# Optimization experiments

Hardware: AMD Instinct MI355X
Metric: run time of the kernel (lower is better)

Reference implementation:

```python
import jax, jax.numpy as jnp
import numpy as np

N_OUT, D_OUT, N_IN, D_IN, N_ROUTING = 32, 32, 2048, 16, 3
BATCH = 64


def squash(x, axis=-1):
    norm2 = jnp.sum(x * x, axis=axis, keepdims=True)
    scale = norm2 / (1.0 + norm2) / jnp.sqrt(norm2)
    return scale * x


def setup_inputs() -> dict:
    key = jax.random.key(0)
    k_u, k_w = jax.random.split(key)
    u = jax.random.normal(k_u, (BATCH, N_IN, D_IN), dtype=jnp.float32)
    stdv = 1.0 / np.sqrt(N_IN)
    W = jax.random.uniform(k_w, (N_IN, D_IN, N_OUT * D_OUT), dtype=jnp.float32,
                           minval=-stdv, maxval=stdv)
    return {"u": u, "W": W}


def reference(u, W):
    B = u.shape[0]
    # uhat[b,n,o,k] = sum_i u[b,n,i] * W[n,i,o*k]
    uhat = jnp.einsum('bni,nij->bnj', u, W).reshape(B, N_IN, N_OUT, D_OUT)
    b = jnp.zeros((B, N_IN, N_OUT), dtype=u.dtype)
    v = None
    for r in range(N_ROUTING):
        c = jax.nn.softmax(b, axis=-1)            # [B, nIn, nOut]
        s = jnp.einsum('bno,bnok->bok', c, uhat)  # [B, nOut, dOut]
        v = squash(s)
        if r != N_ROUTING - 1:
            a = jnp.einsum('bnok,bok->bno', uhat, v)  # agreement
            b = b + a
    return v
```

## Files before the change

kernel.cpp:

```cpp
#include <hip/hip_runtime.h>
#include <math.h>

#define N_OUT 32
#define D_OUT 32
#define N_IN 2048
#define D_IN 16
#define BATCH 64
#define J 1024

typedef __attribute__((ext_vector_type(8))) short short8;
typedef __attribute__((ext_vector_type(4))) float f32x4;

__device__ __forceinline__ unsigned short f2bf(float f) {
  unsigned int x = __float_as_uint(f);
  return (unsigned short)((x + 0x7FFFu + ((x >> 16) & 1u)) >> 16);
}

__device__ __forceinline__ int wp(int u) { return u ^ ((u >> 3) & 1); }

__device__ __forceinline__ void pack_col(const float* wc, uint4& d0, uint4& d1) {
  d0.x = (unsigned)f2bf(wc[0])  | ((unsigned)f2bf(wc[1])  << 16);
  d0.y = (unsigned)f2bf(wc[2])  | ((unsigned)f2bf(wc[3])  << 16);
  d0.z = (unsigned)f2bf(wc[4])  | ((unsigned)f2bf(wc[5])  << 16);
  d0.w = (unsigned)f2bf(wc[6])  | ((unsigned)f2bf(wc[7])  << 16);
  d1.x = (unsigned)f2bf(wc[8])  | ((unsigned)f2bf(wc[9])  << 16);
  d1.y = (unsigned)f2bf(wc[10]) | ((unsigned)f2bf(wc[11]) << 16);
  d1.z = (unsigned)f2bf(wc[12]) | ((unsigned)f2bf(wc[13]) << 16);
  d1.w = (unsigned)f2bf(wc[14]) | ((unsigned)f2bf(wc[15]) << 16);
}

template<bool HAS_V, int MODE, int NCHUNK>
__global__ __launch_bounds__(1024, 1)
void pass_kernel(const float* __restrict__ uf, const float* __restrict__ Wf,
                 short* __restrict__ Wbf, short* __restrict__ ubf,
                 const float* __restrict__ vin, float* __restrict__ part)
{
  constexpr int NBUF = (MODE == 1) ? 4 : 2;
  __shared__ uint4 Wt[NBUF][2048];
  __shared__ float al[2][2][32][18];

  const int t  = threadIdx.x;
  const int l  = t & 63;
  const int w  = t >> 6;
  const int bid = blockIdx.x;
  const int bq = (bid >> 3) & 3;
  const int cx = (bid & 7) | ((bid >> 5) << 3);
  const int n0 = cx * NCHUNK;

  const int bl = l & 15;
  const int b  = bq * 16 + bl;
  const int h  = l >> 4;
  const int hA = h & 1;
  const bool ld = (l < 32);

  f32x4 vf[4];
  if (HAS_V) {
    #pragma unroll
    for (int q = 0; q < 4; ++q)
      vf[q] = *reinterpret_cast<const f32x4*>(vin + (size_t)b * J + (w*4+q)*16 + h*4);
  }

  int aoff[4];
  #pragma unroll
  for (int q = 0; q < 4; ++q) aoff[q] = wp(2 * ((w*4+q) * 16 + bl) + hA);

  f32x4 acc[4];
  #pragma unroll
  for (int q = 0; q < 4; ++q) acc[q] = f32x4{0.f, 0.f, 0.f, 0.f};

  if constexpr (MODE == 1) {
    constexpr int NS = NCHUNK / 2;
    short8 Ba = short8{0,0,0,0,0,0,0,0}, Bb = short8{0,0,0,0,0,0,0,0};
    {
      const uint4* srcA = reinterpret_cast<const uint4*>(Wbf + (size_t)n0 * (D_IN * J));
      Wt[0][t] = srcA[t];
      Wt[0][t + 1024] = srcA[t + 1024];
      const uint4* srcB = reinterpret_cast<const uint4*>(Wbf + (size_t)(n0 + 1) * (D_IN * J));
      Wt[1][t] = srcB[t];
      Wt[1][t + 1024] = srcB[t + 1024];
      if (ld) {
        Ba = *reinterpret_cast<const short8*>(ubf + ((size_t)b * N_IN + n0) * D_IN + hA * 8);
        Bb = *reinterpret_cast<const short8*>(ubf + ((size_t)b * N_IN + n0 + 1) * D_IN + hA * 8);
      }
    }
    __syncthreads();

    for (int ss = 0; ss < NS; ++ss) {
      const int na = n0 + 2 * ss;
      const int p = ss & 1;
      const int par = ss & 1;
      const bool more = (ss + 1 < NS);

      uint4 sa0, sa1, sb0, sb1;
      short8 Bna = short8{0,0,0,0,0,0,0,0}, Bnb = short8{0,0,0,0,0,0,0,0};
      if (more) {
        const uint4* srcA = reinterpret_cast<const uint4*>(Wbf + (size_t)(na + 2) * (D_IN * J));
        sa0 = srcA[t];
        sa1 = srcA[t + 1024];
        const uint4* srcB = reinterpret_cast<const uint4*>(Wbf + (size_t)(na + 3) * (D_IN * J));
        sb0 = srcB[t];
        sb1 = srcB[t + 1024];
        if (ld) {
          Bna = *reinterpret_cast<const short8*>(ubf + ((size_t)b * N_IN + na + 2) * D_IN + hA * 8);
          Bnb = *reinterpret_cast<const short8*>(ubf + ((size_t)b * N_IN + na + 3) * D_IN + hA * 8);
        }
        __builtin_amdgcn_sched_barrier(0);
      }

      f32x4 Ca[4], Cb[4];
      {
        const uint4* bufA = Wt[2 * p];
        const uint4* bufB = Wt[2 * p + 1];
        #pragma unroll
        for (int q = 0; q < 4; ++q) {
          short8 A = short8{0,0,0,0,0,0,0,0};
          if (ld) A = *reinterpret_cast<const short8*>(&bufA[aoff[q]]);
          f32x4 z = f32x4{0.f, 0.f, 0.f, 0.f};
          Ca[q] = __builtin_amdgcn_mfma_f32_16x16x32_bf16(A, Ba, z, 0, 0, 0);
        }
        #pragma unroll
        for (int q = 0; q < 4; ++q) {
          short8 A = short8{0,0,0,0,0,0,0,0};
          if (ld) A = *reinterpret_cast<const short8*>(&bufB[aoff[q]]);
          f32x4 z = f32x4{0.f, 0.f, 0.f, 0.f};
          Cb[q] = __builtin_amdgcn_mfma_f32_16x16x32_bf16(A, Bb, z, 0, 0, 0);
        }
      }

      {
        float apa[2] = {0.f, 0.f}, apb[2] = {0.f, 0.f};
        #pragma unroll
        for (int q = 0; q < 4; ++q) {
          apa[q >> 1] += Ca[q][0]*vf[q][0] + Ca[q][1]*vf[q][1] + Ca[q][2]*vf[q][2] + Ca[q][3]*vf[q][3];
          apb[q >> 1] += Cb[q][0]*vf[q][0] + Cb[q][1]*vf[q][1] + Cb[q][2]*vf[q][2] + Cb[q][3]*vf[q][3];
        }
        #pragma unroll
        for (int p2 = 0; p2 < 2; ++p2) {
          float sa = apa[p2], sb = apb[p2];
          sa += __shfl_xor(sa, 16);
          sa += __shfl_xor(sa, 32);
          sb += __shfl_xor(sb, 16);
          sb += __shfl_xor(sb, 32);
          if (l < 16) {
            al[par][0][w * 2 + p2][l] = sa;
            al[par][1][w * 2 + p2][l] = sb;
          }
        }
      }

      if (more) {
        Wt[2 * (1 - p)][t] = sa0;
        Wt[2 * (1 - p)][t + 1024] = sa1;
        Wt[2 * (1 - p) + 1][t] = sb0;
        Wt[2 * (1 - p) + 1][t + 1024] = sb1;
      }

      __syncthreads();
      {
        int npair = t >> 9, sb2 = (t >> 5) & 15, so = t & 31;
        float x = al[par][npair][so][sb2];
        float m = x;
        #pragma unroll
        for (int k = 1; k < 32; k <<= 1) m = fmaxf(m, __shfl_xor(m, k));
        float e = __expf(x - m);
        float sm = e;
        #pragma unroll
        for (int k = 1; k < 32; k <<= 1) sm += __shfl_xor(sm, k);
        al[par][npair][so][sb2] = e / sm;
      }
      __syncthreads();
      #pragma unroll
      for (int q = 0; q < 4; ++q) {
        float ca = al[par][0][(w * 4 + q) >> 1][bl];
        float cb = al[par][1][(w * 4 + q) >> 1][bl];
        acc[q] += Ca[q] * ca + Cb[q] * cb;
      }
      Ba = Bna;
      Bb = Bnb;
    }
  } else {
    const bool wq = (MODE == 0) && ((t >> 8) == bq);
    const bool uq = (MODE == 0) && (w == 0) && ld;

    short8 Bcur = short8{0,0,0,0,0,0,0,0};
    {
      float wc[16];
      const float* wsrc = Wf + (size_t)n0 * (D_IN * J) + t;
      #pragma unroll
      for (int i = 0; i < 16; ++i) wc[i] = wsrc[i * J];
      float4 a4 = {0,0,0,0}, b4 = {0,0,0,0};
      if (ld) {
        const float* up = uf + ((size_t)b * N_IN + n0) * D_IN + hA * 8;
        a4 = *reinterpret_cast<const float4*>(up);
        b4 = *reinterpret_cast<const float4*>(up + 4);
      }
      __builtin_amdgcn_sched_barrier(0);
      uint4 d0, d1;
      pack_col(wc, d0, d1);
      Wt[0][wp(2 * t)] = d0;
      Wt[0][wp(2 * t + 1)] = d1;
      if (wq) {
        uint4* gdst = reinterpret_cast<uint4*>(Wbf + (size_t)n0 * (D_IN * J));
        gdst[wp(2 * t)] = d0;
        gdst[wp(2 * t + 1)] = d1;
      }
      if (ld) {
        Bcur[0] = (short)f2bf(a4.x); Bcur[1] = (short)f2bf(a4.y);
        Bcur[2] = (short)f2bf(a4.z); Bcur[3] = (short)f2bf(a4.w);
        Bcur[4] = (short)f2bf(b4.x); Bcur[5] = (short)f2bf(b4.y);
        Bcur[6] = (short)f2bf(b4.z); Bcur[7] = (short)f2bf(b4.w);
        if (uq)
          *reinterpret_cast<short8*>(ubf + ((size_t)b * N_IN + n0) * D_IN + hA * 8) = Bcur;
      }
    }
    __syncthreads();

    for (int nn = 0; nn < NCHUNK; ++nn) {
      const int n = n0 + nn;
      const int cur = nn & 1, nxt = cur ^ 1, par = nn & 1;
      const bool more = (nn + 1 < NCHUNK);

      float wc[16];
      float4 a4 = {0,0,0,0}, b4 = {0,0,0,0};
      if (more) {
        const float* wsrc = Wf + (size_t)(n + 1) * (D_IN * J) + t;
        #pragma unroll
        for (int i = 0; i < 16; ++i) wc[i] = wsrc[i * J];
        if (ld) {
          const float* up = uf + ((size_t)b * N_IN + n + 1) * D_IN + hA * 8;
          a4 = *reinterpret_cast<const float4*>(up);
          b4 = *reinterpret_cast<const float4*>(up + 4);
        }
        __builtin_amdgcn_sched_barrier(0);
      }

      f32x4 C[4];
      const uint4* buf = Wt[cur];
      #pragma unroll
      for (int q = 0; q < 4; ++q) {
        short8 A = short8{0,0,0,0,0,0,0,0};
        if (ld) A = *reinterpret_cast<const short8*>(&buf[aoff[q]]);
        f32x4 z = f32x4{0.f, 0.f, 0.f, 0.f};
        C[q] = __builtin_amdgcn_mfma_f32_16x16x32_bf16(A, Bcur, z, 0, 0, 0);
      }

      short8 Bn = short8{0,0,0,0,0,0,0,0};
      if (more && ld) {
        Bn[0] = (short)f2bf(a4.x); Bn[1] = (short)f2bf(a4.y);
        Bn[2] = (short)f2bf(a4.z); Bn[3] = (short)f2bf(a4.w);
        Bn[4] = (short)f2bf(b4.x); Bn[5] = (short)f2bf(b4.y);
        Bn[6] = (short)f2bf(b4.z); Bn[7] = (short)f2bf(b4.w);
      }

      if (HAS_V) {
        float ap[2] = {0.f, 0.f};
        #pragma unroll
        for (int q = 0; q < 4; ++q) {
          float s = C[q][0]*vf[q][0] + C[q][1]*vf[q][1] + C[q][2]*vf[q][2] + C[q][3]*vf[q][3];
          ap[q >> 1] += s;
        }
        #pragma unroll
        for (int p = 0; p < 2; ++p) {
          float s = ap[p];
          s += __shfl_xor(s, 16);
          s += __shfl_xor(s, 32);
          if (l < 16) al[par][0][w * 2 + p][l] = s;
        }
        if (more) {
          uint4 d0, d1;
          pack_col(wc, d0, d1);
          Wt[nxt][wp(2 * t)] = d0;
          Wt[nxt][wp(2 * t + 1)] = d1;
          if (wq) {
            uint4* gdst = reinterpret_cast<uint4*>(Wbf + (size_t)(n + 1) * (D_IN * J));
            gdst[wp(2 * t)] = d0;
            gdst[wp(2 * t + 1)] = d1;
          }
          if (ld && uq)
            *reinterpret_cast<short8*>(ubf + ((size_t)b * N_IN + n + 1) * D_IN + hA * 8) = Bn;
        }
        __syncthreads();
        if (t < 512) {
          int sb = t >> 5, so = t & 31;
          float x = al[par][0][so][sb];
          float m = x;
          #pragma unroll
          for (int k = 1; k < 32; k <<= 1) m = fmaxf(m, __shfl_xor(m, k));
          float e = __expf(x - m);
          float sm = e;
          #pragma unroll
          for (int k = 1; k < 32; k <<= 1) sm += __shfl_xor(sm, k);
          al[par][0][so][sb] = e / sm;
        }
        __syncthreads();
        #pragma unroll
        for (int q = 0; q < 4; ++q) {
          float c = al[par][0][(w * 4 + q) >> 1][bl];
          acc[q] += C[q] * c;
        }
      } else {
        #pragma unroll
        for (int q = 0; q < 4; ++q) acc[q] += C[q];
        if (more) {
          uint4 d0, d1;
          pack_col(wc, d0, d1);
          Wt[nxt][wp(2 * t)] = d0;
          Wt[nxt][wp(2 * t + 1)] = d1;
          if (wq) {
            uint4* gdst = reinterpret_cast<uint4*>(Wbf + (size_t)(n + 1) * (D_IN * J));
            gdst[wp(2 * t)] = d0;
            gdst[wp(2 * t + 1)] = d1;
          }
          if (ld && uq)
            *reinterpret_cast<short8*>(ubf + ((size_t)b * N_IN + n + 1) * D_IN + hA * 8) = Bn;
        }
        __syncthreads();
      }
      Bcur = Bn;
    }
  }

  #pragma unroll
  for (int q = 0; q < 4; ++q) {
    int jbase = (w * 4 + q) * 16 + h * 4;
    #pragma unroll
    for (int r = 0; r < 4; ++r)
      part[((size_t)cx * J + jbase + r) * 64 + b] = acc[q][r];
  }
}

template<int NC>
__global__ __launch_bounds__(1024)
void rsq_kernel(const float* __restrict__ part, const float* __restrict__ addv,
                float* __restrict__ out, float prescale)
{
  __shared__ float ps[2][32][17];
  __shared__ float vl[32][17];
  __shared__ float scl[16];
  const int o  = blockIdx.x >> 2;
  const int bq = blockIdx.x & 3;
  const int t  = threadIdx.x;
  {
    const int bb = t & 15;
    const int kk = (t >> 4) & 31;
    const int ch = t >> 9;
    const float* p = part + (size_t)(o * 32 + kk) * 64 + bq * 16 + bb;
    float s = 0.f;
    #pragma unroll 8
    for (int c = ch * (NC / 2); c < (ch + 1) * (NC / 2); ++c)
      s += p[(size_t)c * (J * 64)];
    ps[ch][kk][bb] = s;
  }
  __syncthreads();
  if (t < 512) {
    int kk = t >> 4, bb = t & 15;
    vl[kk][bb] = (ps[0][kk][bb] + ps[1][kk][bb]) * prescale;
  }
  __syncthreads();
  if (t < 16) {
    float n2 = 0.f;
    #pragma unroll
    for (int k = 0; k < 32; ++k) { float x = vl[k][t]; n2 += x * x; }
    scl[t] = sqrtf(n2) / (1.f + n2);
  }
  __syncthreads();
  if (t < 512) {
    int bb = t >> 5, kk = t & 31;
    int idx = (bq * 16 + bb) * J + o * 32 + kk;
    float val = scl[bb] * vl[kk][bb];
    if (addv) val += addv[idx];
    out[idx] = val;
  }
}

extern "C" void kernel_launch(void* const* d_in, const int* in_sizes, int n_in,
                              void* d_out, int out_size, void* d_ws, size_t ws_size,
                              hipStream_t stream)
{
  const float* u = (const float*)d_in[0];
  const float* W = (const float*)d_in[1];
  float* out = (float*)d_out;
  char* ws = (char*)d_ws;

  const size_t WBF_B = (size_t)N_IN * D_IN * J * 2;
  const size_t UBF_B = (size_t)BATCH * N_IN * D_IN * 2;
  const size_t SMALL = 2ull * BATCH * J * 4;
  const size_t PART64 = (size_t)64 * J * 64 * 4;

  if (ws_size >= WBF_B + UBF_B + PART64 + SMALL) {
    short* Wbf = (short*)ws;
    short* ubf = (short*)(ws + WBF_B);
    float* part = (float*)(ws + WBF_B + UBF_B);
    float* v0 = part + (size_t)64 * J * 64;
    float* vs = v0 + BATCH * J;
    pass_kernel<false, 0, 32><<<256, 1024, 0, stream>>>(u, W, Wbf, ubf, nullptr, part);
    rsq_kernel<64><<<128, 1024, 0, stream>>>(part, nullptr, v0, 1.f / 32.f);
    pass_kernel<true, 1, 32><<<256, 1024, 0, stream>>>(u, W, Wbf, ubf, v0, part);
    rsq_kernel<64><<<128, 1024, 0, stream>>>(part, v0, vs, 1.f);
    pass_kernel<true, 1, 32><<<256, 1024, 0, stream>>>(u, W, Wbf, ubf, vs, part);
    rsq_kernel<64><<<128, 1024, 0, stream>>>(part, nullptr, out, 1.f);
  } else if (ws_size >= PART64 + SMALL) {
    float* part = (float*)ws;
    float* v0 = part + (size_t)64 * J * 64;
    float* vs = v0 + BATCH * J;
    pass_kernel<false, 2, 32><<<256, 1024, 0, stream>>>(u, W, nullptr, nullptr, nullptr, part);
    rsq_kernel<64><<<128, 1024, 0, stream>>>(part, nullptr, v0, 1.f / 32.f);
    pass_kernel<true, 2, 32><<<256, 1024, 0, stream>>>(u, W, nullptr, nullptr, v0, part);
    rsq_kernel<64><<<128, 1024, 0, stream>>>(part, v0, vs, 1.f);
    pass_kernel<true, 2, 32><<<256, 1024, 0, stream>>>(u, W, nullptr, nullptr, vs, part);
    rsq_kernel<64><<<128, 1024, 0, stream>>>(part, nullptr, out, 1.f);
  } else {
    float* part = (float*)ws;
    float* v0 = part + (size_t)16 * J * 64;
    float* vs = v0 + BATCH * J;
    pass_kernel<false, 2, 128><<<64, 1024, 0, stream>>>(u, W, nullptr, nullptr, nullptr, part);
    rsq_kernel<16><<<128, 1024, 0, stream>>>(part, nullptr, v0, 1.f / 32.f);
    pass_kernel<true, 2, 128><<<64, 1024, 0, stream>>>(u, W, nullptr, nullptr, v0, part);
    rsq_kernel<16><<<128, 1024, 0, stream>>>(part, v0, vs, 1.f);
    pass_kernel<true, 2, 128><<<64, 1024, 0, stream>>>(u, W, nullptr, nullptr, vs, part);
    rsq_kernel<16><<<128, 1024, 0, stream>>>(part, nullptr, out, 1.f);
  }
}
```

Measured before the change: 182.6 us.

## Add dedicated first-pass kernel with per-block partials over all batches

Adds a specialized pass0 kernel for the first routing iteration, where the coupling coefficients are uniform. Each of 256 blocks now handles 8 input capsules for all 64 batches, instead of splitting batches across blocks. It converts W to bf16 once per capsule and writes 256 partial sums, which a wider rsq reduction then combines. This removes redundant W loads and conversions across batch quarters, at the cost of a larger partial buffer, a bigger reduction and a higher workspace requirement, with a fallback to the old path.

```diff
diff --git a/kernel.cpp b/kernel.cpp
--- a/kernel.cpp
+++ b/kernel.cpp
@@ -27,6 +27,126 @@
   d1.y = (unsigned)f2bf(wc[10]) | ((unsigned)f2bf(wc[11]) << 16);
   d1.z = (unsigned)f2bf(wc[12]) | ((unsigned)f2bf(wc[13]) << 16);
   d1.w = (unsigned)f2bf(wc[14]) | ((unsigned)f2bf(wc[15]) << 16);
+}
+
+template<int MODE>
+__global__ __launch_bounds__(1024, 1)
+void pass0_kernel(const float* __restrict__ uf, const float* __restrict__ Wf,
+                  short* __restrict__ Wbf, short* __restrict__ ubf,
+                  float* __restrict__ part)
+{
+  __shared__ uint4 Wt[2][2048];
+  const int t  = threadIdx.x;
+  const int l  = t & 63;
+  const int w  = t >> 6;
+  const int cx = blockIdx.x;
+  const int n0 = cx * 8;
+  const int bl = l & 15;
+  const int h  = l >> 4;
+  const int hA = h & 1;
+  const bool ld = (l < 32);
+
+  int aoff[4];
+  #pragma unroll
+  for (int q = 0; q < 4; ++q) aoff[q] = wp(2 * ((w*4+q) * 16 + bl) + hA);
+
+  f32x4 acc[4][4];
+  #pragma unroll
+  for (int bq = 0; bq < 4; ++bq)
+    #pragma unroll
+    for (int q = 0; q < 4; ++q) acc[bq][q] = f32x4{0.f, 0.f, 0.f, 0.f};
+
+  {
+    float wc[16];
+    const float* wsrc = Wf + (size_t)n0 * (D_IN * J) + t;
+    #pragma unroll
+    for (int i = 0; i < 16; ++i) wc[i] = wsrc[i * J];
+    __builtin_amdgcn_sched_barrier(0);
+    uint4 d0, d1;
+    pack_col(wc, d0, d1);
+    Wt[0][wp(2 * t)] = d0;
+    Wt[0][wp(2 * t + 1)] = d1;
+    if (MODE == 0) {
+      uint4* gdst = reinterpret_cast<uint4*>(Wbf + (size_t)n0 * (D_IN * J));
+      gdst[wp(2 * t)] = d0;
+      gdst[wp(2 * t + 1)] = d1;
+    }
+  }
+  __syncthreads();
+
+  for (int nn = 0; nn < 8; ++nn) {
+    const int n = n0 + nn;
+    const int cur = nn & 1, nxt = cur ^ 1;
+    const bool more = (nn + 1 < 8);
+
+    float4 ua[4], ub[4];
+    if (ld) {
+      #pragma unroll
+      for (int bq = 0; bq < 4; ++bq) {
+        const float* up = uf + ((size_t)(bq * 16 + bl) * N_IN + n) * D_IN + hA * 8;
+        ua[bq] = *reinterpret_cast<const float4*>(up);
+        ub[bq] = *reinterpret_cast<const float4*>(up + 4);
+      }
+    }
+    float wc[16];
+    if (more) {
+      const float* wsrc = Wf + (size_t)(n + 1) * (D_IN * J) + t;
+      #pragma unroll
+      for (int i = 0; i < 16; ++i) wc[i] = wsrc[i * J];
+    }
+    __builtin_amdgcn_sched_barrier(0);
+
+    short8 Bq[4];
+    #pragma unroll
+    for (int bq = 0; bq < 4; ++bq) Bq[bq] = short8{0,0,0,0,0,0,0,0};
+    if (ld) {
+      #pragma unroll
+      for (int bq = 0; bq < 4; ++bq) {
+        Bq[bq][0] = (short)f2bf(ua[bq].x); Bq[bq][1] = (short)f2bf(ua[bq].y);
+        Bq[bq][2] = (short)f2bf(ua[bq].z); Bq[bq][3] = (short)f2bf(ua[bq].w);
+        Bq[bq][4] = (short)f2bf(ub[bq].x); Bq[bq][5] = (short)f2bf(ub[bq].y);
+        Bq[bq][6] = (short)f2bf(ub[bq].z); Bq[bq][7] = (short)f2bf(ub[bq].w);
+      }
+      if (MODE == 0 && w == 0) {
+        #pragma unroll
+        for (int bq = 0; bq < 4; ++bq)
+          *reinterpret_cast<short8*>(ubf + ((size_t)(bq * 16 + bl) * N_IN + n) * D_IN + hA * 8) = Bq[bq];
+      }
+    }
+
+    const uint4* buf = Wt[cur];
+    #pragma unroll
+    for (int q = 0; q < 4; ++q) {
+      short8 A = short8{0,0,0,0,0,0,0,0};
+      if (ld) A = *reinterpret_cast<const short8*>(&buf[aoff[q]]);
+      #pragma unroll
+      for (int bq = 0; bq < 4; ++bq)
+        acc[bq][q] = __builtin_amdgcn_mfma_f32_16x16x32_bf16(A, Bq[bq], acc[bq][q], 0, 0, 0);
+    }
+
+    if (more) {
+      uint4 d0, d1;
+      pack_col(wc, d0, d1);
+      Wt[nxt][wp(2 * t)] = d0;
+      Wt[nxt][wp(2 * t + 1)] = d1;
+      if (MODE == 0) {
+        uint4* gdst = reinterpret_cast<uint4*>(Wbf + (size_t)(n + 1) * (D_IN * J));
+        gdst[wp(2 * t)] = d0;
+        gdst[wp(2 * t + 1)] = d1;
+      }
+    }
+    __syncthreads();
+  }
+
+  #pragma unroll
+  for (int bq = 0; bq < 4; ++bq)
+    #pragma unroll
+    for (int q = 0; q < 4; ++q) {
+      int jbase = (w * 4 + q) * 16 + h * 4;
+      #pragma unroll
+      for (int r = 0; r < 4; ++r)
+        part[((size_t)cx * J + jbase + r) * 64 + bq * 16 + bl] = acc[bq][q][r];
+    }
 }
 
 template<bool HAS_V, int MODE, int NCHUNK>
@@ -385,9 +505,22 @@
   const size_t WBF_B = (size_t)N_IN * D_IN * J * 2;
   const size_t UBF_B = (size_t)BATCH * N_IN * D_IN * 2;
   const size_t SMALL = 2ull * BATCH * J * 4;
-  const size_t PART64 = (size_t)64 * J * 64 * 4;
-
-  if (ws_size >= WBF_B + UBF_B + PART64 + SMALL) {
+  const size_t PART256 = (size_t)256 * J * 64 * 4;
+  const size_t PART64  = (size_t)64 * J * 64 * 4;
+
+  if (ws_size >= WBF_B + UBF_B + PART256 + SMALL) {
+    short* Wbf = (short*)ws;
+    short* ubf = (short*)(ws + WBF_B);
+    float* part = (float*)(ws + WBF_B + UBF_B);
+    float* v0 = part + (size_t)256 * J * 64;
+    float* vs = v0 + BATCH * J;
+    pass0_kernel<0><<<256, 1024, 0, stream>>>(u, W, Wbf, ubf, part);
+    rsq_kernel<256><<<128, 1024, 0, stream>>>(part, nullptr, v0, 1.f / 32.f);
+    pass_kernel<true, 1, 32><<<256, 1024, 0, stream>>>(u, W, Wbf, ubf, v0, part);
+    rsq_kernel<64><<<128, 1024, 0, stream>>>(part, v0, vs, 1.f);
+    pass_kernel<true, 1, 32><<<256, 1024, 0, stream>>>(u, W, Wbf, ubf, vs, part);
+    rsq_kernel<64><<<128, 1024, 0, stream>>>(part, nullptr, out, 1.f);
+  } else if (ws_size >= WBF_B + UBF_B + PART64 + SMALL) {
     short* Wbf = (short*)ws;
     short* ubf = (short*)(ws + WBF_B);
     float* part = (float*)(ws + WBF_B + UBF_B);
```

New measurement: 320.7 us. 1.76x slower.

## Add dedicated first-pass kernel processing two input capsules per barrier step

Applied to the files above, without the earlier changes.

Adds a specialized kernel for the first routing pass that loads, converts and stages two input capsules per iteration into a four-slot shared-memory ring. It accumulates the MFMA products across the chunk instead of doing per-capsule reductions, then writes partial sums once at the end. This halves the number of block-wide barriers and deepens the prefetch. In exchange it uses more registers for twice the in-flight global loads and double the shared-memory staging.

```diff
diff --git a/kernel.cpp b/kernel.cpp
--- a/kernel.cpp
+++ b/kernel.cpp
@@ -27,6 +27,180 @@
   d1.y = (unsigned)f2bf(wc[10]) | ((unsigned)f2bf(wc[11]) << 16);
   d1.z = (unsigned)f2bf(wc[12]) | ((unsigned)f2bf(wc[13]) << 16);
   d1.w = (unsigned)f2bf(wc[14]) | ((unsigned)f2bf(wc[15]) << 16);
+}
+
+__device__ __forceinline__ short8 pack_u(const float4& a4, const float4& b4) {
+  short8 B;
+  B[0] = (short)f2bf(a4.x); B[1] = (short)f2bf(a4.y);
+  B[2] = (short)f2bf(a4.z); B[3] = (short)f2bf(a4.w);
+  B[4] = (short)f2bf(b4.x); B[5] = (short)f2bf(b4.y);
+  B[6] = (short)f2bf(b4.z); B[7] = (short)f2bf(b4.w);
+  return B;
+}
+
+template<int MODE>
+__global__ __launch_bounds__(1024, 1)
+void pass0p_kernel(const float* __restrict__ uf, const float* __restrict__ Wf,
+                   short* __restrict__ Wbf, short* __restrict__ ubf,
+                   float* __restrict__ part)
+{
+  __shared__ uint4 Wt[4][2048];
+
+  const int t  = threadIdx.x;
+  const int l  = t & 63;
+  const int w  = t >> 6;
+  const int bid = blockIdx.x;
+  const int bq = (bid >> 3) & 3;
+  const int cx = (bid & 7) | ((bid >> 5) << 3);
+  const int n0 = cx * 32;
+
+  const int bl = l & 15;
+  const int b  = bq * 16 + bl;
+  const int h  = l >> 4;
+  const int hA = h & 1;
+  const bool ld = (l < 32);
+  const bool wq = (MODE == 0) && ((t >> 8) == bq);
+  const bool uq = (MODE == 0) && (w == 0) && ld;
+
+  int aoff[4];
+  #pragma unroll
+  for (int q = 0; q < 4; ++q) aoff[q] = wp(2 * ((w*4+q) * 16 + bl) + hA);
+
+  f32x4 acc[4];
+  #pragma unroll
+  for (int q = 0; q < 4; ++q) acc[q] = f32x4{0.f, 0.f, 0.f, 0.f};
+
+  short8 Ba = short8{0,0,0,0,0,0,0,0}, Bb = short8{0,0,0,0,0,0,0,0};
+
+  {
+    float wa[16], wb[16];
+    const float* sa = Wf + (size_t)n0 * (D_IN * J) + t;
+    const float* sb = Wf + (size_t)(n0 + 1) * (D_IN * J) + t;
+    #pragma unroll
+    for (int i = 0; i < 16; ++i) wa[i] = sa[i * J];
+    #pragma unroll
+    for (int i = 0; i < 16; ++i) wb[i] = sb[i * J];
+    float4 ua0 = {0,0,0,0}, ua1 = {0,0,0,0}, ub0 = {0,0,0,0}, ub1 = {0,0,0,0};
+    if (ld) {
+      const float* upa = uf + ((size_t)b * N_IN + n0) * D_IN + hA * 8;
+      ua0 = *reinterpret_cast<const float4*>(upa);
+      ua1 = *reinterpret_cast<const float4*>(upa + 4);
+      const float* upb = uf + ((size_t)b * N_IN + n0 + 1) * D_IN + hA * 8;
+      ub0 = *reinterpret_cast<const float4*>(upb);
+      ub1 = *reinterpret_cast<const float4*>(upb + 4);
+    }
+    __builtin_amdgcn_sched_barrier(0);
+    uint4 d0, d1;
+    pack_col(wa, d0, d1);
+    Wt[0][wp(2 * t)] = d0;
+    Wt[0][wp(2 * t + 1)] = d1;
+    if (wq) {
+      uint4* g = reinterpret_cast<uint4*>(Wbf + (size_t)n0 * (D_IN * J));
+      g[wp(2 * t)] = d0;
+      g[wp(2 * t + 1)] = d1;
+    }
+    pack_col(wb, d0, d1);
+    Wt[1][wp(2 * t)] = d0;
+    Wt[1][wp(2 * t + 1)] = d1;
+    if (wq) {
+      uint4* g = reinterpret_cast<uint4*>(Wbf + (size_t)(n0 + 1) * (D_IN * J));
+      g[wp(2 * t)] = d0;
+      g[wp(2 * t + 1)] = d1;
+    }
+    if (ld) {
+      Ba = pack_u(ua0, ua1);
+      Bb = pack_u(ub0, ub1);
+      if (uq) {
+        *reinterpret_cast<short8*>(ubf + ((size_t)b * N_IN + n0) * D_IN + hA * 8) = Ba;
+        *reinterpret_cast<short8*>(ubf + ((size_t)b * N_IN + n0 + 1) * D_IN + hA * 8) = Bb;
+      }
+    }
+  }
+  __syncthreads();
+
+  for (int ss = 0; ss < 16; ++ss) {
+    const int na = n0 + 2 * ss;
+    const int p = ss & 1;
+    const bool more = (ss + 1 < 16);
+
+    float wa[16], wb[16];
+    float4 ua0 = {0,0,0,0}, ua1 = {0,0,0,0}, ub0 = {0,0,0,0}, ub1 = {0,0,0,0};
+    if (more) {
+      const float* sa = Wf + (size_t)(na + 2) * (D_IN * J) + t;
+      const float* sb = Wf + (size_t)(na + 3) * (D_IN * J) + t;
+      #pragma unroll
+      for (int i = 0; i < 16; ++i) wa[i] = sa[i * J];
+      #pragma unroll
+      for (int i = 0; i < 16; ++i) wb[i] = sb[i * J];
+      if (ld) {
+        const float* upa = uf + ((size_t)b * N_IN + na + 2) * D_IN + hA * 8;
+        ua0 = *reinterpret_cast<const float4*>(upa);
+        ua1 = *reinterpret_cast<const float4*>(upa + 4);
+        const float* upb = uf + ((size_t)b * N_IN + na + 3) * D_IN + hA * 8;
+        ub0 = *reinterpret_cast<const float4*>(upb);
+        ub1 = *reinterpret_cast<const float4*>(upb + 4);
+      }
+      __builtin_amdgcn_sched_barrier(0);
+    }
+
+    {
+      const uint4* bufA = Wt[2 * p];
+      const uint4* bufB = Wt[2 * p + 1];
+      #pragma unroll
+      for (int q = 0; q < 4; ++q) {
+        short8 A = short8{0,0,0,0,0,0,0,0};
+        if (ld) A = *reinterpret_cast<const short8*>(&bufA[aoff[q]]);
+        acc[q] = __builtin_amdgcn_mfma_f32_16x16x32_bf16(A, Ba, acc[q], 0, 0, 0);
+      }
+      #pragma unroll
+      for (int q = 0; q < 4; ++q) {
+        short8 A = short8{0,0,0,0,0,0,0,0};
+        if (ld) A = *reinterpret_cast<const short8*>(&bufB[aoff[q]]);
+        acc[q] = __builtin_amdgcn_mfma_f32_16x16x32_bf16(A, Bb, acc[q], 0, 0, 0);
+      }
+    }
+
+    short8 Bna = short8{0,0,0,0,0,0,0,0}, Bnb = short8{0,0,0,0,0,0,0,0};
+    if (more) {
+      uint4 d0, d1;
+      pack_col(wa, d0, d1);
+      Wt[2 * (1 - p)][wp(2 * t)] = d0;
+      Wt[2 * (1 - p)][wp(2 * t + 1)] = d1;
+      if (wq) {
+        uint4* g = reinterpret_cast<uint4*>(Wbf + (size_t)(na + 2) * (D_IN * J));
+        g[wp(2 * t)] = d0;
+        g[wp(2 * t + 1)] = d1;
+      }
+      pack_col(wb, d0, d1);
+      Wt[2 * (1 - p) + 1][wp(2 * t)] = d0;
+      Wt[2 * (1 - p) + 1][wp(2 * t + 1)] = d1;
+      if (wq) {
+        uint4* g = reinterpret_cast<uint4*>(Wbf + (size_t)(na + 3) * (D_IN * J));
+        g[wp(2 * t)] = d0;
+        g[wp(2 * t + 1)] = d1;
+      }
+      if (ld) {
+        Bna = pack_u(ua0, ua1);
+        Bnb = pack_u(ub0, ub1);
+        if (uq) {
+          *reinterpret_cast<short8*>(ubf + ((size_t)b * N_IN + na + 2) * D_IN + hA * 8) = Bna;
+          *reinterpret_cast<short8*>(ubf + ((size_t)b * N_IN + na + 3) * D_IN + hA * 8) = Bnb;
+        }
+      }
+    }
+
+    __syncthreads();
+    Ba = Bna;
+    Bb = Bnb;
+  }
+
+  #pragma unroll
+  for (int q = 0; q < 4; ++q) {
+    int jbase = (w * 4 + q) * 16 + h * 4;
+    #pragma unroll
+    for (int r = 0; r < 4; ++r)
+      part[((size_t)cx * J + jbase + r) * 64 + b] = acc[q][r];
+  }
 }
 
 template<bool HAS_V, int MODE, int NCHUNK>
@@ -205,10 +379,7 @@
         gdst[wp(2 * t + 1)] = d1;
       }
       if (ld) {
-        Bcur[0] = (short)f2bf(a4.x); Bcur[1] = (short)f2bf(a4.y);
-        Bcur[2] = (short)f2bf(a4.z); Bcur[3] = (short)f2bf(a4.w);
-        Bcur[4] = (short)f2bf(b4.x); Bcur[5] = (short)f2bf(b4.y);
-        Bcur[6] = (short)f2bf(b4.z); Bcur[7] = (short)f2bf(b4.w);
+        Bcur = pack_u(a4, b4);
         if (uq)
           *reinterpret_cast<short8*>(ubf + ((size_t)b * N_IN + n0) * D_IN + hA * 8) = Bcur;
       }
@@ -245,12 +416,7 @@
       }
 
       short8 Bn = short8{0,0,0,0,0,0,0,0};
-      if (more && ld) {
-        Bn[0] = (short)f2bf(a4.x); Bn[1] = (short)f2bf(a4.y);
-        Bn[2] = (short)f2bf(a4.z); Bn[3] = (short)f2bf(a4.w);
-        Bn[4] = (short)f2bf(b4.x); Bn[5] = (short)f2bf(b4.y);
-        Bn[6] = (short)f2bf(b4.z); Bn[7] = (short)f2bf(b4.w);
-      }
+      if (more && ld) Bn = pack_u(a4, b4);
 
       if (HAS_V) {
         float ap[2] = {0.f, 0.f};
@@ -393,7 +559,7 @@
     float* part = (float*)(ws + WBF_B + UBF_B);
     float* v0 = part + (size_t)64 * J * 64;
     float* vs = v0 + BATCH * J;
-    pass_kernel<false, 0, 32><<<256, 1024, 0, stream>>>(u, W, Wbf, ubf, nullptr, part);
+    pass0p_kernel<0><<<256, 1024, 0, stream>>>(u, W, Wbf, ubf, part);
     rsq_kernel<64><<<128, 1024, 0, stream>>>(part, nullptr, v0, 1.f / 32.f);
     pass_kernel<true, 1, 32><<<256, 1024, 0, stream>>>(u, W, Wbf, ubf, v0, part);
     rsq_kernel<64><<<128, 1024, 0, stream>>>(part, v0, vs, 1.f);
```

After: 180.0 us. No clear change (-1.4%).
